# Optimization experiments

Measured on AMD Instinct MI355X. Metric: run time of the kernel, lower is better.

The kernel has to match this reference:

```python
import jax, jax.numpy as jnp
from jax import lax
import numpy as np

WIN = (9, 9, 9)
NUM_CH = 5       # Ii, Ji, I2, J2, IJ stacked on channel dim, grouped conv


def setup_inputs() -> dict:
    key = jax.random.key(0)
    k1, k2 = jax.random.split(key)
    shape = (1, 1, 128, 160, 192)
    y_true = jax.random.uniform(k1, shape, dtype=jnp.float32)
    y_pred = jax.random.uniform(k2, shape, dtype=jnp.float32)
    return {"y_true": y_true, "y_pred": y_pred}


def _box_sum_3d(x, win):
    # x: [B, 5, D, H, W]
    for ax, k in enumerate(win):
        kshape = [NUM_CH, 1, 1, 1, 1]
        kshape[2 + ax] = k
        kernel = jnp.ones(kshape, x.dtype)
        pads = [(0, 0)] * 3
        pads[ax] = (k // 2, k // 2)
        x = lax.conv_general_dilated(
            x, kernel, window_strides=(1, 1, 1), padding=pads,
            dimension_numbers=("NCDHW", "OIDHW", "NCDHW"),
            feature_group_count=NUM_CH)
    return x


def reference(y_true, y_pred):
    Ii, Ji = y_true, y_pred
    stacked = jnp.concatenate([Ii, Ji, Ii * Ii, Ji * Ji, Ii * Ji], axis=1)  # [B,5,D,H,W]
    sums = _box_sum_3d(stacked, WIN)
    I_sum, J_sum, I2_sum, J2_sum, IJ_sum = jnp.split(sums, NUM_CH, axis=1)
    win_size = float(np.prod(WIN))
    cross = IJ_sum - J_sum / win_size * I_sum
    I_var = I2_sum - I_sum / win_size * I_sum
    J_var = J2_sum - J_sum / win_size * J_sum
    cc = cross * cross / (I_var * J_var + 1e-05)
    return 1.0 - jnp.mean(cc)
```

## Files before the change

kernel.cpp:

```cpp
#include <hip/hip_runtime.h>
#include <hip/hip_fp16.h>


#define D_ 128
#define H_ 160
#define W_ 192
#define WP_ (W_ / 2)
#define HW_ (H_ * W_)
#define HWP_ (HW_ / 2)
#define N_ (D_ * H_ * W_)
#define NP_ (N_ / 2)
#define WIN_INV (1.0f / 729.0f)
#define HR2 10
#define CH3 8

__device__ __forceinline__ unsigned pack2(float x, float y) {
    __half2 h = __float22half2_rn(make_float2(x, y));
    return *reinterpret_cast<unsigned*>(&h);
}
__device__ __forceinline__ float2 unpack2(unsigned u) {
    __half2 h = *reinterpret_cast<__half2*>(&u);
    return __half22float2(h);
}

__device__ __forceinline__ void addU(float2 S[5], const uint4& q, unsigned sv) {
    float2 v0 = unpack2(q.x), v1 = unpack2(q.y), v2 = unpack2(q.z),
           v3 = unpack2(q.w), v4 = unpack2(sv);
    S[0].x += v0.x; S[0].y += v0.y;
    S[1].x += v1.x; S[1].y += v1.y;
    S[2].x += v2.x; S[2].y += v2.y;
    S[3].x += v3.x; S[3].y += v3.y;
    S[4].x += v4.x; S[4].y += v4.y;
}
__device__ __forceinline__ void subU(float2 S[5], const uint4& q, unsigned sv) {
    float2 v0 = unpack2(q.x), v1 = unpack2(q.y), v2 = unpack2(q.z),
           v3 = unpack2(q.w), v4 = unpack2(sv);
    S[0].x -= v0.x; S[0].y -= v0.y;
    S[1].x -= v1.x; S[1].y -= v1.y;
    S[2].x -= v2.x; S[2].y -= v2.y;
    S[3].x -= v3.x; S[3].y -= v3.y;
    S[4].x -= v4.x; S[4].y -= v4.y;
}

__global__ __launch_bounds__(256) void ncc_pass1(const float* __restrict__ I,
                                                 const float* __restrict__ J,
                                                 uint4* __restrict__ Aq,
                                                 unsigned* __restrict__ As,
                                                 float* __restrict__ acc) {
    __shared__ float sI[2 * W_];
    __shared__ float sJ[2 * W_];
    const int t = threadIdx.x;
    const int line0 = blockIdx.x * 2;
    const int base = line0 * W_;
    sI[t] = I[base + t];
    sJ[t] = J[base + t];
    if (t < 2 * W_ - 256) { sI[t + 256] = I[base + t + 256]; sJ[t + 256] = J[base + t + 256]; }
    if (blockIdx.x == 0 && t == 0) *acc = 0.0f;
    __syncthreads();
    if (t >= 2 * WP_) return;
    const int ll = t / WP_;
    const int wp = t % WP_;
    const int w0 = 2 * wp;
    const float* a_ = sI + ll * W_;
    const float* b_ = sJ + ll * W_;
    float s1a = 0, s2a = 0, s3a = 0, s4a = 0, s5a = 0;
    float s1b = 0, s2b = 0, s3b = 0, s4b = 0, s5b = 0;
#pragma unroll
    for (int j = -4; j <= 5; ++j) {
        int idx = w0 + j;
        float a = 0.f, b = 0.f;
        if (idx >= 0 && idx < W_) { a = a_[idx]; b = b_[idx]; }
        float p3 = a * a, p4 = b * b, p5 = a * b;
        if (j <= 4) { s1a += a; s2a += b; s3a += p3; s4a += p4; s5a += p5; }
        if (j >= -3) { s1b += a; s2b += b; s3b += p3; s4b += p4; s5b += p5; }
    }
    const size_t o = (size_t)(line0 + ll) * WP_ + wp;
    Aq[o] = make_uint4(pack2(s1a, s1b), pack2(s2a, s2b),
                       pack2(s3a, s3b), pack2(s4a, s4b));
    As[o] = pack2(s5a, s5b);
}

__global__ __launch_bounds__(256) void ncc_pass2(const uint4* __restrict__ Aq,
                                                 const unsigned* __restrict__ As,
                                                 uint4* __restrict__ Bq,
                                                 unsigned* __restrict__ Bs) {
    const int t = blockIdx.x * 256 + threadIdx.x;
    const int wp = t % WP_;
    const int r = t / WP_;
    const int hc = r & 15;
    const int d = r >> 4;
    const size_t cb = (size_t)d * (H_ * WP_) + wp;
    const uint4* aq = Aq + cb;
    const unsigned* as_ = As + cb;
    uint4* bq = Bq + cb;
    unsigned* bs = Bs + cb;
    const int h0 = hc * HR2;

    uint4 fq[9]; unsigned fs[9];
    float2 S[5] = {{0,0},{0,0},{0,0},{0,0},{0,0}};
#pragma unroll
    for (int j = 0; j < 9; ++j) {
        int hh = h0 - 4 + j;
        uint4 q = make_uint4(0u, 0u, 0u, 0u); unsigned sv = 0u;
        if ((unsigned)hh < (unsigned)H_) {
            q = aq[(size_t)hh * WP_]; sv = as_[(size_t)hh * WP_];
        }
        fq[j] = q; fs[j] = sv;
        addU(S, q, sv);
    }
#pragma unroll
    for (int i = 0; i < HR2; ++i) {
        const int h = h0 + i;
        bq[(size_t)h * WP_] = make_uint4(pack2(S[0].x, S[0].y), pack2(S[1].x, S[1].y),
                                         pack2(S[2].x, S[2].y), pack2(S[3].x, S[3].y));
        bs[(size_t)h * WP_] = pack2(S[4].x, S[4].y);
        if (i + 1 < HR2) {
            int hh = h + 5;
            uint4 q = make_uint4(0u, 0u, 0u, 0u); unsigned sv = 0u;
            if (hh < H_) { q = aq[(size_t)hh * WP_]; sv = as_[(size_t)hh * WP_]; }
            subU(S, fq[0], fs[0]);
            addU(S, q, sv);
#pragma unroll
            for (int j = 0; j < 8; ++j) { fq[j] = fq[j + 1]; fs[j] = fs[j + 1]; }
            fq[8] = q; fs[8] = sv;
        }
    }
}

__global__ __launch_bounds__(256) void ncc_pass3(const uint4* __restrict__ Bq,
                                                 const unsigned* __restrict__ Bs,
                                                 float* __restrict__ acc) {
    const int pp = (blockIdx.x % (HWP_ / 256)) * 256 + threadIdx.x;
    const int d0 = (blockIdx.x / (HWP_ / 256)) * CH3;
    const uint4* bq = Bq + pp;
    const unsigned* bs = Bs + pp;

    uint4 fq[9]; unsigned fs[9];
    float2 S[5] = {{0,0},{0,0},{0,0},{0,0},{0,0}};
#pragma unroll
    for (int j = 0; j < 9; ++j) {
        int dd = d0 - 4 + j;
        uint4 q = make_uint4(0u, 0u, 0u, 0u); unsigned sv = 0u;
        if ((unsigned)dd < (unsigned)D_) {
            q = bq[(size_t)dd * HWP_]; sv = bs[(size_t)dd * HWP_];
        }
        fq[j] = q; fs[j] = sv;
        addU(S, q, sv);
    }
    float sum = 0.f;
#pragma unroll
    for (int i = 0; i < CH3; ++i) {
        {
            float cr = S[4].x - S[1].x * S[0].x * WIN_INV;
            float Iv = S[2].x - S[0].x * S[0].x * WIN_INV;
            float Jv = S[3].x - S[1].x * S[1].x * WIN_INV;
            sum += cr * cr / (Iv * Jv + 1e-5f);
        }
        {
            float cr = S[4].y - S[1].y * S[0].y * WIN_INV;
            float Iv = S[2].y - S[0].y * S[0].y * WIN_INV;
            float Jv = S[3].y - S[1].y * S[1].y * WIN_INV;
            sum += cr * cr / (Iv * Jv + 1e-5f);
        }
        if (i + 1 < CH3) {
            int dl = d0 + i + 5;
            uint4 q = make_uint4(0u, 0u, 0u, 0u); unsigned sv = 0u;
            if (dl < D_) { q = bq[(size_t)dl * HWP_]; sv = bs[(size_t)dl * HWP_]; }
            subU(S, fq[0], fs[0]);
            addU(S, q, sv);
#pragma unroll
            for (int j = 0; j < 8; ++j) { fq[j] = fq[j + 1]; fs[j] = fs[j + 1]; }
            fq[8] = q; fs[8] = sv;
        }
    }

    for (int off = 32; off; off >>= 1) sum += __shfl_down(sum, off, 64);
    __shared__ float wsum[4];
    const int lane = threadIdx.x & 63, wv = threadIdx.x >> 6;
    if (lane == 0) wsum[wv] = sum;
    __syncthreads();
    if (threadIdx.x == 0)
        atomicAdd(acc, wsum[0] + wsum[1] + wsum[2] + wsum[3]);
}

__global__ void ncc_finalize(const float* __restrict__ acc,
                             float* __restrict__ out) {
    out[0] = 1.0f - acc[0] * (1.0f / (float)N_);
}

extern "C" void kernel_launch(void* const* d_in, const int* in_sizes, int n_in,
                              void* d_out, int out_size, void* d_ws, size_t ws_size,
                              hipStream_t stream) {
    const float* I = (const float*)d_in[0];
    const float* J = (const float*)d_in[1];
    char* w = (char*)d_ws;
    uint4* Aq = (uint4*)w;
    uint4* Bq = (uint4*)(w + (size_t)NP_ * 16);
    unsigned* As = (unsigned*)(w + (size_t)NP_ * 32);
    unsigned* Bs = (unsigned*)(w + (size_t)NP_ * 36);
    float* acc = (float*)(w + (size_t)NP_ * 40);
    float* out = (float*)d_out;

    ncc_pass1<<<D_ * H_ / 2, 256, 0, stream>>>(I, J, Aq, As, acc);
    ncc_pass2<<<(D_ * 16 * WP_) / 256, 256, 0, stream>>>(Aq, As, Bq, Bs);
    ncc_pass3<<<(HWP_ / 256) * (D_ / CH3), 256, 0, stream>>>(Bq, Bs, acc);
    ncc_finalize<<<1, 1, 0, stream>>>(acc, out);
}
```

Before: 54.53 us.

## Accumulate sliding window sums in packed half2 and fuse finalize into pass3

Pass2 and pass3 now keep their sliding-window sums as packed __half2 and use __hadd2/__hsub2 directly on the stored fp16 data, instead of unpacking to float and repacking. This removes the conversion instructions from the inner loops. In exchange, running sums of squares over up to 729 elements are kept in fp16, which adds rounding error and could overflow near the fp16 maximum. The separate finalize kernel is also dropped: the last pass3 block, found through an atomic counter, writes the output, saving one kernel launch.

```diff
diff --git a/kernel.cpp b/kernel.cpp
--- a/kernel.cpp
+++ b/kernel.cpp
@@ -13,40 +13,21 @@
 #define WIN_INV (1.0f / 729.0f)
 #define HR2 10
 #define CH3 8
-
+#define NBLK3 ((HWP_ / 256) * (D_ / CH3))
+
+union U32H2 { unsigned u; __half2 h; };
+__device__ __forceinline__ __half2 u2h(unsigned u) { U32H2 x; x.u = u; return x.h; }
+__device__ __forceinline__ unsigned h2u(__half2 h) { U32H2 x; x.h = h; return x.u; }
 __device__ __forceinline__ unsigned pack2(float x, float y) {
-    __half2 h = __float22half2_rn(make_float2(x, y));
-    return *reinterpret_cast<unsigned*>(&h);
-}
-__device__ __forceinline__ float2 unpack2(unsigned u) {
-    __half2 h = *reinterpret_cast<__half2*>(&u);
-    return __half22float2(h);
-}
-
-__device__ __forceinline__ void addU(float2 S[5], const uint4& q, unsigned sv) {
-    float2 v0 = unpack2(q.x), v1 = unpack2(q.y), v2 = unpack2(q.z),
-           v3 = unpack2(q.w), v4 = unpack2(sv);
-    S[0].x += v0.x; S[0].y += v0.y;
-    S[1].x += v1.x; S[1].y += v1.y;
-    S[2].x += v2.x; S[2].y += v2.y;
-    S[3].x += v3.x; S[3].y += v3.y;
-    S[4].x += v4.x; S[4].y += v4.y;
-}
-__device__ __forceinline__ void subU(float2 S[5], const uint4& q, unsigned sv) {
-    float2 v0 = unpack2(q.x), v1 = unpack2(q.y), v2 = unpack2(q.z),
-           v3 = unpack2(q.w), v4 = unpack2(sv);
-    S[0].x -= v0.x; S[0].y -= v0.y;
-    S[1].x -= v1.x; S[1].y -= v1.y;
-    S[2].x -= v2.x; S[2].y -= v2.y;
-    S[3].x -= v3.x; S[3].y -= v3.y;
-    S[4].x -= v4.x; S[4].y -= v4.y;
+    return h2u(__float22half2_rn(make_float2(x, y)));
 }
 
 __global__ __launch_bounds__(256) void ncc_pass1(const float* __restrict__ I,
                                                  const float* __restrict__ J,
                                                  uint4* __restrict__ Aq,
                                                  unsigned* __restrict__ As,
-                                                 float* __restrict__ acc) {
+                                                 float* __restrict__ acc,
+                                                 unsigned* __restrict__ ctr) {
     __shared__ float sI[2 * W_];
     __shared__ float sJ[2 * W_];
     const int t = threadIdx.x;
@@ -55,7 +36,7 @@
     sI[t] = I[base + t];
     sJ[t] = J[base + t];
     if (t < 2 * W_ - 256) { sI[t + 256] = I[base + t + 256]; sJ[t + 256] = J[base + t + 256]; }
-    if (blockIdx.x == 0 && t == 0) *acc = 0.0f;
+    if (blockIdx.x == 0 && t == 0) { *acc = 0.0f; *ctr = 0u; }
     __syncthreads();
     if (t >= 2 * WP_) return;
     const int ll = t / WP_;
@@ -97,7 +78,8 @@
     const int h0 = hc * HR2;
 
     uint4 fq[9]; unsigned fs[9];
-    float2 S[5] = {{0,0},{0,0},{0,0},{0,0},{0,0}};
+    const __half2 z = __float2half2_rn(0.f);
+    __half2 S0 = z, S1 = z, S2 = z, S3 = z, S4 = z;
 #pragma unroll
     for (int j = 0; j < 9; ++j) {
         int hh = h0 - 4 + j;
@@ -106,20 +88,24 @@
             q = aq[(size_t)hh * WP_]; sv = as_[(size_t)hh * WP_];
         }
         fq[j] = q; fs[j] = sv;
-        addU(S, q, sv);
+        S0 = __hadd2(S0, u2h(q.x)); S1 = __hadd2(S1, u2h(q.y));
+        S2 = __hadd2(S2, u2h(q.z)); S3 = __hadd2(S3, u2h(q.w));
+        S4 = __hadd2(S4, u2h(sv));
     }
 #pragma unroll
     for (int i = 0; i < HR2; ++i) {
         const int h = h0 + i;
-        bq[(size_t)h * WP_] = make_uint4(pack2(S[0].x, S[0].y), pack2(S[1].x, S[1].y),
-                                         pack2(S[2].x, S[2].y), pack2(S[3].x, S[3].y));
-        bs[(size_t)h * WP_] = pack2(S[4].x, S[4].y);
+        bq[(size_t)h * WP_] = make_uint4(h2u(S0), h2u(S1), h2u(S2), h2u(S3));
+        bs[(size_t)h * WP_] = h2u(S4);
         if (i + 1 < HR2) {
             int hh = h + 5;
             uint4 q = make_uint4(0u, 0u, 0u, 0u); unsigned sv = 0u;
             if (hh < H_) { q = aq[(size_t)hh * WP_]; sv = as_[(size_t)hh * WP_]; }
-            subU(S, fq[0], fs[0]);
-            addU(S, q, sv);
+            S0 = __hadd2(__hsub2(S0, u2h(fq[0].x)), u2h(q.x));
+            S1 = __hadd2(__hsub2(S1, u2h(fq[0].y)), u2h(q.y));
+            S2 = __hadd2(__hsub2(S2, u2h(fq[0].z)), u2h(q.z));
+            S3 = __hadd2(__hsub2(S3, u2h(fq[0].w)), u2h(q.w));
+            S4 = __hadd2(__hsub2(S4, u2h(fs[0])), u2h(sv));
 #pragma unroll
             for (int j = 0; j < 8; ++j) { fq[j] = fq[j + 1]; fs[j] = fs[j + 1]; }
             fq[8] = q; fs[8] = sv;
@@ -129,14 +115,17 @@
 
 __global__ __launch_bounds__(256) void ncc_pass3(const uint4* __restrict__ Bq,
                                                  const unsigned* __restrict__ Bs,
-                                                 float* __restrict__ acc) {
+                                                 float* __restrict__ acc,
+                                                 unsigned* __restrict__ ctr,
+                                                 float* __restrict__ out) {
     const int pp = (blockIdx.x % (HWP_ / 256)) * 256 + threadIdx.x;
     const int d0 = (blockIdx.x / (HWP_ / 256)) * CH3;
     const uint4* bq = Bq + pp;
     const unsigned* bs = Bs + pp;
 
     uint4 fq[9]; unsigned fs[9];
-    float2 S[5] = {{0,0},{0,0},{0,0},{0,0},{0,0}};
+    const __half2 z = __float2half2_rn(0.f);
+    __half2 S0 = z, S1 = z, S2 = z, S3 = z, S4 = z;
 #pragma unroll
     for (int j = 0; j < 9; ++j) {
         int dd = d0 - 4 + j;
@@ -145,29 +134,37 @@
             q = bq[(size_t)dd * HWP_]; sv = bs[(size_t)dd * HWP_];
         }
         fq[j] = q; fs[j] = sv;
-        addU(S, q, sv);
+        S0 = __hadd2(S0, u2h(q.x)); S1 = __hadd2(S1, u2h(q.y));
+        S2 = __hadd2(S2, u2h(q.z)); S3 = __hadd2(S3, u2h(q.w));
+        S4 = __hadd2(S4, u2h(sv));
     }
     float sum = 0.f;
 #pragma unroll
     for (int i = 0; i < CH3; ++i) {
+        const float2 s0 = __half22float2(S0), s1 = __half22float2(S1),
+                     s2 = __half22float2(S2), s3 = __half22float2(S3),
+                     s4 = __half22float2(S4);
         {
-            float cr = S[4].x - S[1].x * S[0].x * WIN_INV;
-            float Iv = S[2].x - S[0].x * S[0].x * WIN_INV;
-            float Jv = S[3].x - S[1].x * S[1].x * WIN_INV;
+            float cr = s4.x - s1.x * s0.x * WIN_INV;
+            float Iv = s2.x - s0.x * s0.x * WIN_INV;
+            float Jv = s3.x - s1.x * s1.x * WIN_INV;
             sum += cr * cr / (Iv * Jv + 1e-5f);
         }
         {
-            float cr = S[4].y - S[1].y * S[0].y * WIN_INV;
-            float Iv = S[2].y - S[0].y * S[0].y * WIN_INV;
-            float Jv = S[3].y - S[1].y * S[1].y * WIN_INV;
+            float cr = s4.y - s1.y * s0.y * WIN_INV;
+            float Iv = s2.y - s0.y * s0.y * WIN_INV;
+            float Jv = s3.y - s1.y * s1.y * WIN_INV;
             sum += cr * cr / (Iv * Jv + 1e-5f);
         }
         if (i + 1 < CH3) {
             int dl = d0 + i + 5;
             uint4 q = make_uint4(0u, 0u, 0u, 0u); unsigned sv = 0u;
             if (dl < D_) { q = bq[(size_t)dl * HWP_]; sv = bs[(size_t)dl * HWP_]; }
-            subU(S, fq[0], fs[0]);
-            addU(S, q, sv);
+            S0 = __hadd2(__hsub2(S0, u2h(fq[0].x)), u2h(q.x));
+            S1 = __hadd2(__hsub2(S1, u2h(fq[0].y)), u2h(q.y));
+            S2 = __hadd2(__hsub2(S2, u2h(fq[0].z)), u2h(q.z));
+            S3 = __hadd2(__hsub2(S3, u2h(fq[0].w)), u2h(q.w));
+            S4 = __hadd2(__hsub2(S4, u2h(fs[0])), u2h(sv));
 #pragma unroll
             for (int j = 0; j < 8; ++j) { fq[j] = fq[j + 1]; fs[j] = fs[j + 1]; }
             fq[8] = q; fs[8] = sv;
@@ -179,13 +176,15 @@
     const int lane = threadIdx.x & 63, wv = threadIdx.x >> 6;
     if (lane == 0) wsum[wv] = sum;
     __syncthreads();
-    if (threadIdx.x == 0)
+    if (threadIdx.x == 0) {
         atomicAdd(acc, wsum[0] + wsum[1] + wsum[2] + wsum[3]);
-}
-
-__global__ void ncc_finalize(const float* __restrict__ acc,
-                             float* __restrict__ out) {
-    out[0] = 1.0f - acc[0] * (1.0f / (float)N_);
+        __threadfence();
+        unsigned t = atomicAdd(ctr, 1u);
+        if (t == NBLK3 - 1) {
+            float v = atomicAdd(acc, 0.0f);
+            out[0] = 1.0f - v * (1.0f / (float)N_);
+        }
+    }
 }
 
 extern "C" void kernel_launch(void* const* d_in, const int* in_sizes, int n_in,
@@ -199,10 +198,10 @@
     unsigned* As = (unsigned*)(w + (size_t)NP_ * 32);
     unsigned* Bs = (unsigned*)(w + (size_t)NP_ * 36);
     float* acc = (float*)(w + (size_t)NP_ * 40);
+    unsigned* ctr = (unsigned*)(w + (size_t)NP_ * 40 + 4);
     float* out = (float*)d_out;
 
-    ncc_pass1<<<D_ * H_ / 2, 256, 0, stream>>>(I, J, Aq, As, acc);
+    ncc_pass1<<<D_ * H_ / 2, 256, 0, stream>>>(I, J, Aq, As, acc, ctr);
     ncc_pass2<<<(D_ * 16 * WP_) / 256, 256, 0, stream>>>(Aq, As, Bq, Bs);
-    ncc_pass3<<<(HWP_ / 256) * (D_ / CH3), 256, 0, stream>>>(Bq, Bs, acc);
-    ncc_finalize<<<1, 1, 0, stream>>>(acc, out);
-}
+    ncc_pass3<<<NBLK3, 256, 0, stream>>>(Bq, Bs, acc, ctr, out);
+}
```

After: 75.05 us. 37.6% more time.
